# Kernel tuning notes

Hardware: AMD Instinct MI355X
Metric: run time of the kernel (lower is better)

## Reference

```python
import jax, jax.numpy as jnp
import numpy as np

B, DIM, L, S, E = 4096, 3, 300, 60, 128
P = L // S  # points per local region = 5


def setup_inputs() -> dict:
    key = jax.random.key(0)
    ks = jax.random.split(key, 9)
    inp = {
        "x": jax.random.normal(ks[0], (B, DIM, L), dtype=jnp.float32),
        # local_emb_nn: Conv1d(DIM, E, 1) -> weight [E, DIM], bias [E]
        "W_le": jax.random.normal(ks[1], (E, DIM), dtype=jnp.float32) * 0.1,
        "b_le": jax.random.normal(ks[2], (E,), dtype=jnp.float32) * 0.1,
        "W_lr": jax.random.normal(ks[3], (S, P), dtype=jnp.float32) * 0.1,
        "b_lr": jax.random.normal(ks[4], (S,), dtype=jnp.float32) * 0.1,
        # global_emb_nn: Conv1d(DIM, E, 1)
        "W_ge": jax.random.normal(ks[5], (E, DIM), dtype=jnp.float32) * 0.1,
        "b_ge": jax.random.normal(ks[6], (E,), dtype=jnp.float32) * 0.1,
        # global_nn: Conv1d(L, 1, 1) -> weight [L], bias scalar
        "W_gn": jax.random.normal(ks[7], (L,), dtype=jnp.float32) * 0.1,
        "b_gn": jax.random.normal(ks[8], (), dtype=jnp.float32) * 0.1,
    }
    return inp


def reference(x, W_le, b_le, W_lr, b_lr, W_ge, b_ge, W_gn, b_gn):
    # global branch: [B,DIM,L] -> [B,E,L] -> relu -> transpose [B,L,E]
    gf = jax.nn.relu(jnp.einsum('ec,bcl->ble', W_ge, x) + b_ge)
    # global_nn: 1x1 conv over L channels -> [B,E], then relu
    gf = jax.nn.relu(jnp.einsum('l,ble->be', W_gn, gf) + b_gn)
    # local branch: [B,DIM,L] -> [B,E,L] -> relu -> transpose [B,L,E]
    lf = jax.nn.relu(jnp.einsum('ec,bcl->ble', W_le, x) + b_le)
    # chunk into S regions of P points, apply per-region 1x1 conv (P->1)
    lf = lf.reshape(B, S, P, E)
    lf = jnp.einsum('sp,bspe->bse', W_lr, lf) + b_lr[None, :, None]
    # add broadcast global feature [B,1,E]
    return lf + gf[:, None, :]
```

## Files before the change

### kernel.cpp

```cpp
#include <hip/hip_runtime.h>


typedef float v2f __attribute__((ext_vector_type(2)));

#define PKFMA(a, b, c) __builtin_elementwise_fma((a), (b), (c))
#define PKRELU(a)      __builtin_elementwise_max((a), (v2f)0.0f)
#define SPLAT(s)       ((v2f)(s))

__global__ __launch_bounds__(256) void cle_kernel(
    const float* __restrict__ x,
    const float* __restrict__ W_le,
    const float* __restrict__ b_le,
    const float* __restrict__ W_lr,
    const float* __restrict__ b_lr,
    const float* __restrict__ W_ge,
    const float* __restrict__ b_ge,
    const float* __restrict__ W_gn,
    const float* __restrict__ b_gn,
    float* __restrict__ out)
{
    const int tid  = threadIdx.x;
    const int lane = tid & 63;
    const int wq   = __builtin_amdgcn_readfirstlane(tid >> 6);
    const int b    = blockIdx.x;
    const int e0   = lane << 1;

    __shared__ __align__(16) float4 sx4[225];
    __shared__ v2f sgp[4][64];

    if (tid < 225) sx4[tid] = ((const float4*)(x + (size_t)b * 900))[tid];

    const v2f wg0 = {W_ge[e0 * 3 + 0], W_ge[e0 * 3 + 3]};
    const v2f wg1 = {W_ge[e0 * 3 + 1], W_ge[e0 * 3 + 4]};
    const v2f wg2 = {W_ge[e0 * 3 + 2], W_ge[e0 * 3 + 5]};
    const v2f bg  = {b_ge[e0], b_ge[e0 + 1]};
    const v2f wl0 = {W_le[e0 * 3 + 0], W_le[e0 * 3 + 3]};
    const v2f wl1 = {W_le[e0 * 3 + 1], W_le[e0 * 3 + 4]};
    const v2f wl2 = {W_le[e0 * 3 + 2], W_le[e0 * 3 + 5]};
    const v2f bl  = {b_le[e0], b_le[e0 + 1]};
    const float bgn = b_gn[0];

    __syncthreads();

#define GE(cmp) PKRELU(PKFMA(wg2, SPLAT(c2.cmp), PKFMA(wg1, SPLAT(c1.cmp), PKFMA(wg0, SPLAT(c0.cmp), bg))))
#define LE(cmp) PKRELU(PKFMA(wl2, SPLAT(c2.cmp), PKFMA(wl1, SPLAT(c1.cmp), PKFMA(wl0, SPLAT(c0.cmp), bl))))

    v2f ga0 = SPLAT(0.f), ga1 = SPLAT(0.f), ga2 = SPLAT(0.f), ga3 = SPLAT(0.f);
    {
        const int qb = wq * 20;
        const int nq = (wq < 3) ? 20 : 15;
        for (int g = 0; g < 4; ++g) {
            if (g * 5 < nq) {
#pragma unroll
                for (int qi = 0; qi < 5; ++qi) {
                    const int qq = qb + g * 5 + qi;
                    const int l4 = qq * 4;
                    const float4 c0 = sx4[qq], c1 = sx4[75 + qq], c2 = sx4[150 + qq];
                    ga0 = PKFMA(SPLAT(W_gn[l4 + 0]), GE(x), ga0);
                    ga1 = PKFMA(SPLAT(W_gn[l4 + 1]), GE(y), ga1);
                    ga2 = PKFMA(SPLAT(W_gn[l4 + 2]), GE(z), ga2);
                    ga3 = PKFMA(SPLAT(W_gn[l4 + 3]), GE(w), ga3);
                }
            }
        }
    }
    sgp[wq][lane] = (ga0 + ga1) + (ga2 + ga3);
    __syncthreads();

    v2f gf;
    {
        const v2f p0 = sgp[0][lane], p1 = sgp[1][lane];
        const v2f p2 = sgp[2][lane], p3 = sgp[3][lane];
        gf = PKRELU(((p0 + p1) + (p2 + p3)) + SPLAT(bgn));
    }

    v2f* ob2 = (v2f*)(out + (size_t)b * (60 * 128)) + lane;

#define DOQ(qi, A0, A1, A2, A3)                                                \
    {                                                                          \
        const int qq = q0 + (qi);                                              \
        const int lw = qq * 4;                 \
        const float4 c0 = sx4[qq], c1 = sx4[75 + qq], c2 = sx4[150 + qq];      \
        A0 = PKFMA(SPLAT(W_lr[lw + 0]), LE(x), A0);                            \
        A1 = PKFMA(SPLAT(W_lr[lw + 1]), LE(y), A1);                            \
        A2 = PKFMA(SPLAT(W_lr[lw + 2]), LE(z), A2);                            \
        A3 = PKFMA(SPLAT(W_lr[lw + 3]), LE(w), A3);                            \
    }

    {
        const int ng = (wq < 3) ? 4 : 3;
        for (int g = 0; g < 4; ++g) {
            if (g < ng) {
                const int q0 = wq * 20 + g * 5;
                v2f a0 = SPLAT(0.f), a1 = SPLAT(0.f), a2 = SPLAT(0.f), a3 = SPLAT(0.f);
                DOQ(0, a0, a0, a0, a0)
                DOQ(1, a0, a1, a1, a1)
                DOQ(2, a1, a1, a2, a2)
                DOQ(3, a2, a2, a2, a3)
                DOQ(4, a3, a3, a3, a3)

                const int s0 = wq * 16 + g * 4;
                ob2[(s0 + 0) * 64] = a0 + gf + SPLAT(b_lr[s0 + 0]);
                ob2[(s0 + 1) * 64] = a1 + gf + SPLAT(b_lr[s0 + 1]);
                ob2[(s0 + 2) * 64] = a2 + gf + SPLAT(b_lr[s0 + 2]);
                ob2[(s0 + 3) * 64] = a3 + gf + SPLAT(b_lr[s0 + 3]);
            }
        }
    }
}

extern "C" void kernel_launch(void* const* d_in, const int* in_sizes, int n_in,
                              void* d_out, int out_size, void* d_ws, size_t ws_size,
                              hipStream_t stream) {
    const float* x    = (const float*)d_in[0];
    const float* W_le = (const float*)d_in[1];
    const float* b_le = (const float*)d_in[2];
    const float* W_lr = (const float*)d_in[3];
    const float* b_lr = (const float*)d_in[4];
    const float* W_ge = (const float*)d_in[5];
    const float* b_ge = (const float*)d_in[6];
    const float* W_gn = (const float*)d_in[7];
    const float* b_gn = (const float*)d_in[8];
    float* out = (float*)d_out;

    cle_kernel<<<4096, 256, 0, stream>>>(x, W_le, b_le, W_lr, b_lr,
                                         W_ge, b_ge, W_gn, b_gn, out);
}
```

Before: 47.24 us.

## Fuse global and local passes into one loop with five balanced waves

Merges the global-embedding reduction into the local-region loop so each x element is read from LDS once for both branches. The output stores move after the single barrier. Block size goes from 4 to 5 waves so each wave handles 15 quads (12 regions) and the load is balanced. This trades extra live accumulator registers (12 v2f) and delayed stores for less LDS traffic and no idle wave tail.

```diff
diff --git a/kernel.cpp b/kernel.cpp
--- a/kernel.cpp
+++ b/kernel.cpp
@@ -7,7 +7,7 @@
 #define PKRELU(a)      __builtin_elementwise_max((a), (v2f)0.0f)
 #define SPLAT(s)       ((v2f)(s))
 
-__global__ __launch_bounds__(256) void cle_kernel(
+__global__ __launch_bounds__(320) void cle_kernel(
     const float* __restrict__ x,
     const float* __restrict__ W_le,
     const float* __restrict__ b_le,
@@ -26,7 +26,7 @@
     const int e0   = lane << 1;
 
     __shared__ __align__(16) float4 sx4[225];
-    __shared__ v2f sgp[4][64];
+    __shared__ v2f sgp[5][64];
 
     if (tid < 225) sx4[tid] = ((const float4*)(x + (size_t)b * 900))[tid];
 
@@ -45,42 +45,20 @@
 #define GE(cmp) PKRELU(PKFMA(wg2, SPLAT(c2.cmp), PKFMA(wg1, SPLAT(c1.cmp), PKFMA(wg0, SPLAT(c0.cmp), bg))))
 #define LE(cmp) PKRELU(PKFMA(wl2, SPLAT(c2.cmp), PKFMA(wl1, SPLAT(c1.cmp), PKFMA(wl0, SPLAT(c0.cmp), bl))))
 
-    v2f ga0 = SPLAT(0.f), ga1 = SPLAT(0.f), ga2 = SPLAT(0.f), ga3 = SPLAT(0.f);
-    {
-        const int qb = wq * 20;
-        const int nq = (wq < 3) ? 20 : 15;
-        for (int g = 0; g < 4; ++g) {
-            if (g * 5 < nq) {
-#pragma unroll
-                for (int qi = 0; qi < 5; ++qi) {
-                    const int qq = qb + g * 5 + qi;
-                    const int l4 = qq * 4;
-                    const float4 c0 = sx4[qq], c1 = sx4[75 + qq], c2 = sx4[150 + qq];
-                    ga0 = PKFMA(SPLAT(W_gn[l4 + 0]), GE(x), ga0);
-                    ga1 = PKFMA(SPLAT(W_gn[l4 + 1]), GE(y), ga1);
-                    ga2 = PKFMA(SPLAT(W_gn[l4 + 2]), GE(z), ga2);
-                    ga3 = PKFMA(SPLAT(W_gn[l4 + 3]), GE(w), ga3);
-                }
-            }
-        }
-    }
-    sgp[wq][lane] = (ga0 + ga1) + (ga2 + ga3);
-    __syncthreads();
-
-    v2f gf;
-    {
-        const v2f p0 = sgp[0][lane], p1 = sgp[1][lane];
-        const v2f p2 = sgp[2][lane], p3 = sgp[3][lane];
-        gf = PKRELU(((p0 + p1) + (p2 + p3)) + SPLAT(bgn));
-    }
-
-    v2f* ob2 = (v2f*)(out + (size_t)b * (60 * 128)) + lane;
+    v2f ga0 = SPLAT(0.f), ga1 = SPLAT(0.f);
+    v2f A00 = SPLAT(0.f), A01 = SPLAT(0.f), A02 = SPLAT(0.f), A03 = SPLAT(0.f);
+    v2f A10 = SPLAT(0.f), A11 = SPLAT(0.f), A12 = SPLAT(0.f), A13 = SPLAT(0.f);
+    v2f A20 = SPLAT(0.f), A21 = SPLAT(0.f), A22 = SPLAT(0.f), A23 = SPLAT(0.f);
 
 #define DOQ(qi, A0, A1, A2, A3)                                                \
     {                                                                          \
         const int qq = q0 + (qi);                                              \
-        const int lw = qq * 4;                 \
+        const int lw = qq * 4;                          \
         const float4 c0 = sx4[qq], c1 = sx4[75 + qq], c2 = sx4[150 + qq];      \
+        ga0 = PKFMA(SPLAT(W_gn[lw + 0]), GE(x), ga0);                          \
+        ga1 = PKFMA(SPLAT(W_gn[lw + 1]), GE(y), ga1);                          \
+        ga0 = PKFMA(SPLAT(W_gn[lw + 2]), GE(z), ga0);                          \
+        ga1 = PKFMA(SPLAT(W_gn[lw + 3]), GE(w), ga1);                          \
         A0 = PKFMA(SPLAT(W_lr[lw + 0]), LE(x), A0);                            \
         A1 = PKFMA(SPLAT(W_lr[lw + 1]), LE(y), A1);                            \
         A2 = PKFMA(SPLAT(W_lr[lw + 2]), LE(z), A2);                            \
@@ -88,25 +66,54 @@
     }
 
     {
-        const int ng = (wq < 3) ? 4 : 3;
-        for (int g = 0; g < 4; ++g) {
-            if (g < ng) {
-                const int q0 = wq * 20 + g * 5;
-                v2f a0 = SPLAT(0.f), a1 = SPLAT(0.f), a2 = SPLAT(0.f), a3 = SPLAT(0.f);
-                DOQ(0, a0, a0, a0, a0)
-                DOQ(1, a0, a1, a1, a1)
-                DOQ(2, a1, a1, a2, a2)
-                DOQ(3, a2, a2, a2, a3)
-                DOQ(4, a3, a3, a3, a3)
+        const int q0 = wq * 15;
+        DOQ(0, A00, A00, A00, A00)
+        DOQ(1, A00, A01, A01, A01)
+        DOQ(2, A01, A01, A02, A02)
+        DOQ(3, A02, A02, A02, A03)
+        DOQ(4, A03, A03, A03, A03)
+    }
+    {
+        const int q0 = wq * 15 + 5;
+        DOQ(0, A10, A10, A10, A10)
+        DOQ(1, A10, A11, A11, A11)
+        DOQ(2, A11, A11, A12, A12)
+        DOQ(3, A12, A12, A12, A13)
+        DOQ(4, A13, A13, A13, A13)
+    }
+    {
+        const int q0 = wq * 15 + 10;
+        DOQ(0, A20, A20, A20, A20)
+        DOQ(1, A20, A21, A21, A21)
+        DOQ(2, A21, A21, A22, A22)
+        DOQ(3, A22, A22, A22, A23)
+        DOQ(4, A23, A23, A23, A23)
+    }
 
-                const int s0 = wq * 16 + g * 4;
-                ob2[(s0 + 0) * 64] = a0 + gf + SPLAT(b_lr[s0 + 0]);
-                ob2[(s0 + 1) * 64] = a1 + gf + SPLAT(b_lr[s0 + 1]);
-                ob2[(s0 + 2) * 64] = a2 + gf + SPLAT(b_lr[s0 + 2]);
-                ob2[(s0 + 3) * 64] = a3 + gf + SPLAT(b_lr[s0 + 3]);
-            }
-        }
+    sgp[wq][lane] = ga0 + ga1;
+    __syncthreads();
+
+    v2f gf;
+    {
+        const v2f p0 = sgp[0][lane], p1 = sgp[1][lane], p2 = sgp[2][lane];
+        const v2f p3 = sgp[3][lane], p4 = sgp[4][lane];
+        gf = PKRELU((((p0 + p1) + (p2 + p3)) + p4) + SPLAT(bgn));
     }
+
+    v2f* ob2 = (v2f*)(out + (size_t)b * (60 * 128)) + lane;
+    const int s0 = wq * 12;
+    ob2[(s0 +  0) * 64] = A00 + gf + SPLAT(b_lr[s0 +  0]);
+    ob2[(s0 +  1) * 64] = A01 + gf + SPLAT(b_lr[s0 +  1]);
+    ob2[(s0 +  2) * 64] = A02 + gf + SPLAT(b_lr[s0 +  2]);
+    ob2[(s0 +  3) * 64] = A03 + gf + SPLAT(b_lr[s0 +  3]);
+    ob2[(s0 +  4) * 64] = A10 + gf + SPLAT(b_lr[s0 +  4]);
+    ob2[(s0 +  5) * 64] = A11 + gf + SPLAT(b_lr[s0 +  5]);
+    ob2[(s0 +  6) * 64] = A12 + gf + SPLAT(b_lr[s0 +  6]);
+    ob2[(s0 +  7) * 64] = A13 + gf + SPLAT(b_lr[s0 +  7]);
+    ob2[(s0 +  8) * 64] = A20 + gf + SPLAT(b_lr[s0 +  8]);
+    ob2[(s0 +  9) * 64] = A21 + gf + SPLAT(b_lr[s0 +  9]);
+    ob2[(s0 + 10) * 64] = A22 + gf + SPLAT(b_lr[s0 + 10]);
+    ob2[(s0 + 11) * 64] = A23 + gf + SPLAT(b_lr[s0 + 11]);
 }
 
 extern "C" void kernel_launch(void* const* d_in, const int* in_sizes, int n_in,
@@ -123,6 +130,6 @@
     const float* b_gn = (const float*)d_in[8];
     float* out = (float*)d_out;
 
-    cle_kernel<<<4096, 256, 0, stream>>>(x, W_le, b_le, W_lr, b_lr,
+    cle_kernel<<<4096, 320, 0, stream>>>(x, W_le, b_le, W_lr, b_lr,
                                          W_ge, b_ge, W_gn, b_gn, out);
 }
```

Result: no change. 46.72 us (-1.1%).
